# Kernel tuning notes

Hardware: AMD Instinct MI355X
Metric: run time of the kernel (lower is better)

The kernel has to match this reference:

```python
import math
import jax, jax.numpy as jnp
import numpy as np

FACTOR = 5

def setup_inputs() -> dict:
    key = jax.random.key(0)
    kq, kk, kv, ki = jax.random.split(key, 4)
    b, h, L, d = 4, 8, 4096, 64
    sample_k = min(L, int(FACTOR * math.log(L + 1)))  # 41
    q = jax.random.normal(kq, (b, h, L, d), dtype=jnp.float32)
    k = jax.random.normal(kk, (b, h, L, d), dtype=jnp.float32)
    v = jax.random.normal(kv, (b, h, L, d), dtype=jnp.float32)
    index_sample = jax.random.randint(ki, (L, sample_k), 0, L, dtype=jnp.int64)
    return {"q": q, "k": k, "v": v, "index_sample": index_sample}

def reference(q, k, v, index_sample):
    b, h, l_q, d = q.shape
    l_k = k.shape[2]
    n_top = min(l_q, int(FACTOR * math.log(l_q + 1)))
    # --- ProbSparse query selection ---
    # k_sample[b,h,q,s,d] = k[b,h,index_sample[q,s],d]  (avoids the O(lq*lk*d) expand)
    k_sample = k[:, :, index_sample, :]                      # (b,h,l_q,sample_k,d)
    qk_sample = jnp.einsum('bhqd,bhqsd->bhqs', q, k_sample)  # (b,h,l_q,sample_k)
    m = qk_sample.max(axis=-1) - qk_sample.mean(axis=-1)     # sparsity measure
    _, top_q = jax.lax.top_k(m, n_top)                       # (b,h,n_top)
    # --- sparse attention on selected queries ---
    q_reduce = jnp.take_along_axis(q, top_q[..., None], axis=2)  # (b,h,n_top,d)
    scale = 1.0 / math.sqrt(d)
    scores = jnp.einsum('bhnd,bhkd->bhnk', q_reduce, k) * scale
    attn = jax.nn.softmax(scores, axis=-1)
    context_top = jnp.einsum('bhnk,bhkd->bhnd', attn, v)
    # --- scatter into mean-initialized context (attn_mask is None path) ---
    context = jnp.broadcast_to(v.mean(axis=2, keepdims=True), (b, h, l_q, d))
    bi = jnp.arange(b)[:, None, None]
    hi = jnp.arange(h)[None, :, None]
    context = context.at[bi, hi, top_q].set(context_top)
    return context
```

## Files before the change

### kernel.cpp

```cpp
#include <hip/hip_runtime.h>
#include <hip/hip_bf16.h>


#define NTOP 41
#define NPAD 48
#define CH 64
#define CAND_CAP 64

typedef __attribute__((ext_vector_type(8))) short bf16x8;
typedef __attribute__((ext_vector_type(4))) float f32x4;

__device__ __forceinline__ unsigned short f2bf(float f) {
    unsigned int x = __float_as_uint(f);
    unsigned int r = (x + 0x7FFFu + ((x >> 16) & 1u)) >> 16;
    return (unsigned short)r;
}
__device__ __forceinline__ unsigned int pack2(float lo, float hi) {
    return ((unsigned int)f2bf(hi) << 16) | f2bf(lo);
}
__device__ __forceinline__ float dot8(const float4& qa, const float4& qb,
                                      const float4& ka, const float4& kb) {
    float p = 0.f;
    p = fmaf(qa.x, ka.x, p); p = fmaf(qa.y, ka.y, p);
    p = fmaf(qa.z, ka.z, p); p = fmaf(qa.w, ka.w, p);
    p = fmaf(qb.x, kb.x, p); p = fmaf(qb.y, kb.y, p);
    p = fmaf(qb.z, kb.z, p); p = fmaf(qb.w, kb.w, p);
    return p;
}
__device__ __forceinline__ float red8(float p) {
    p += __shfl_xor(p, 1);
    p += __shfl_xor(p, 2);
    p += __shfl_xor(p, 4);
    return p;
}

__global__ __launch_bounds__(256, 5) void K1_scores_vsum(const float* __restrict__ q,
                                                         const float* __restrict__ k,
                                                         const float* __restrict__ v,
                                                         const int* __restrict__ idxs,
                                                         float* __restrict__ m_out,
                                                         float* __restrict__ vpart) {
    __shared__ __align__(16) char smem[32 * 41 * 4 > 1024 ? 32 * 41 * 4 : 1024];
    int t = threadIdx.x;
    int bid = blockIdx.x;

    if (bid < 512) {
        float* red = (float*)smem;
        int bh = bid >> 4, chn = bid & 15;
        int d = t & 63, r = t >> 6;
        long long base = ((long long)bh << 12) + chn * 256;
        float acc = 0.f;
        for (int i = 0; i < 64; i++) acc += v[(base + i * 4 + r) * 64 + d];
        red[t] = acc;
        __syncthreads();
        if (r == 0)
            vpart[(bh * 16 + chn) * 64 + d] = red[d] + red[64 + d] + red[128 + d] + red[192 + d];
        return;
    }

    int* sidx = (int*)smem;
    int abid = bid - 512;
    int lane = t & 63, w = t >> 6;
    int g = lane >> 3, sl = lane & 7;
    int lb = ((abid & 7) << 9) + (abid >> 3);
    long long qflat = (long long)lb * 32 + w * 8 + g;
    int bh = (int)(qflat >> 12);
    int qi0 = (lb * 32) & 4095;
    for (int i = t; i < 32 * 41; i += 256)
        sidx[i] = idxs[(long long)qi0 * 41 + i] & 4095;
    const float4* q4 = (const float4*)q;
    const float4* k4 = (const float4*)k;
    float4 qa = q4[qflat * 16 + sl * 2];
    float4 qb = q4[qflat * 16 + sl * 2 + 1];
    long long kbase = ((long long)bh << 12) * 16;
    __syncthreads();
    const int* irow = sidx + (w * 8 + g) * 41;

    int k40 = irow[40];
    float4 ka40 = k4[kbase + (long long)k40 * 16 + sl * 2];
    float4 kb40 = k4[kbase + (long long)k40 * 16 + sl * 2 + 1];

    float maxv = -1e30f, sum = 0.f;
#pragma unroll
    for (int g8 = 0; g8 < 5; g8++) {
        int kis[8];
#pragma unroll
        for (int u = 0; u < 8; u++) kis[u] = irow[g8 * 8 + u];
        float4 ka[8], kb[8];
#pragma unroll
        for (int u = 0; u < 8; u++) {
            long long roff = kbase + (long long)kis[u] * 16 + sl * 2;
            ka[u] = k4[roff];
            kb[u] = k4[roff + 1];
        }
#pragma unroll
        for (int u = 0; u < 8; u++) {
            float p = red8(dot8(qa, qb, ka[u], kb[u]));
            maxv = fmaxf(maxv, p);
            sum += p;
        }
    }
    {
        float p = red8(dot8(qa, qb, ka40, kb40));
        maxv = fmaxf(maxv, p);
        sum += p;
    }
    if (sl == 0) m_out[qflat] = maxv - sum * (1.0f / 41.0f);
}

__global__ __launch_bounds__(256) void kB_topk(const float* __restrict__ m_in,
                                               int* __restrict__ topq) {
    __shared__ unsigned int uvals[4096];
    __shared__ unsigned int hist[256];
    __shared__ unsigned int scal[4];
    __shared__ int candIdx[CAND_CAP];
    __shared__ unsigned int candU[CAND_CAP];
    int bh = blockIdx.x, t = threadIdx.x;
    for (int i = t; i < 4096; i += 256) {
        unsigned int b = __float_as_uint(m_in[bh * 4096 + i]);
        uvals[i] = (b & 0x80000000u) ? ~b : (b | 0x80000000u);
    }
    hist[t] = 0;
    __syncthreads();
    for (int i = t; i < 4096; i += 256) atomicAdd(&hist[uvals[i] >> 24], 1u);
    __syncthreads();
    if (t == 0) {
        unsigned int cum = 0, b1 = 0, ca = 0;
        for (int j = 255; j >= 0; j--) {
            if (cum + hist[j] >= 41u) { b1 = (unsigned)j; ca = cum; break; }
            cum += hist[j];
        }
        scal[0] = b1; scal[1] = ca;
    }
    __syncthreads();
    unsigned int b1 = scal[0];
    hist[t] = 0;
    __syncthreads();
    for (int i = t; i < 4096; i += 256)
        if ((uvals[i] >> 24) == b1) atomicAdd(&hist[(uvals[i] >> 16) & 255u], 1u);
    __syncthreads();
    if (t == 0) {
        unsigned int cum = scal[1], b2 = 0;
        for (int j = 255; j >= 0; j--) {
            if (cum + hist[j] >= 41u) { b2 = (unsigned)j; break; }
            cum += hist[j];
        }
        scal[2] = (b1 << 24) | (b2 << 16);
        scal[3] = 0;
    }
    __syncthreads();
    unsigned int T = scal[2];
    for (int i = t; i < 4096; i += 256) {
        unsigned int u = uvals[i];
        if (u >= T) {
            unsigned int pos = atomicAdd(&scal[3], 1u);
            if (pos < CAND_CAP) { candIdx[pos] = i; candU[pos] = u; }
        }
    }
    __syncthreads();
    if (t < 64) {
        int n = (int)min(scal[3], (unsigned)CAND_CAP);
        unsigned int myU = (t < n) ? candU[t] : 0u;
        int myI = (t < n) ? candIdx[t] : 0x7fffffff;
        for (int it = 0; it < NTOP; it++) {
            unsigned int bu = myU;
            int bi = myI;
            for (int off = 32; off; off >>= 1) {
                unsigned int ou = __shfl_xor(bu, off);
                int oi = __shfl_xor(bi, off);
                if (ou > bu || (ou == bu && oi < bi)) { bu = ou; bi = oi; }
            }
            if (t == 0) topq[bh * NTOP + it] = bi;
            if (myI == bi) { myU = 0u; myI = 0x7fffffff; }
        }
    }
}

__global__ __launch_bounds__(256) void K3_attn_bcast(const float* __restrict__ q,
                                                     const float* __restrict__ k,
                                                     const float* __restrict__ v,
                                                     const int* __restrict__ topq,
                                                     const float* __restrict__ vpart,
                                                     float* __restrict__ part,
                                                     float* __restrict__ out,
                                                     int tiles, int tl) {
    __shared__ unsigned short qs[NPAD * 72];
    __shared__ unsigned short kb[CH * 72];
    __shared__ unsigned short vt[64 * 72];
    __shared__ unsigned short pb[NPAD * 72];
    __shared__ float sp[NPAD * 65];
    __shared__ float m_i[NPAD], l_i[NPAD], fac[NPAD];
    __shared__ __align__(16) float vm[64];

    const int t = threadIdx.x;
    const int bid = blockIdx.x;
    const int nE = tiles * 32;

    if (bid >= nE) {
        int gb = bid - nE;
        int bh = gb >> 6;
        if (t < 64) {
            float s = 0.f;
#pragma unroll
            for (int c = 0; c < 16; c++) s += vpart[(bh * 16 + c) * 64 + t];
            vm[t] = s * (1.0f / 4096.0f);
        }
        __syncthreads();
        long long g0 = (long long)gb * 1024 + t;
        float4* out4 = (float4*)out;
#pragma unroll
        for (int i = 0; i < 4; i++) {
            long long gg = g0 + i * 256;
            int d4 = (int)(gg & 15);
            out4[gg] = *(const float4*)(&vm[d4 * 4]);
        }
        return;
    }

    const int xcd = bid & 7, sub = (bid >> 3) & 3, tile = bid >> 5;
    const int bh = (xcd << 2) | sub;
    const int lane = t & 63, w = t >> 6;
    const int c = lane & 15, quad = lane >> 4;
    const long long bhbase = ((long long)bh) << 12;

    const float4* q4f = (const float4*)q;
    const float4* k4f = (const float4*)k;
    const float4* v4f = (const float4*)v;

    for (int i = t; i < NTOP * 16; i += 256) {
        int n = i >> 4, oc = i & 15;
        int row = topq[bh * NTOP + n];
        float4 val = q4f[(bhbase + row) * 16 + oc];
        uint2 pk;
        pk.x = pack2(val.x * 0.125f, val.y * 0.125f);
        pk.y = pack2(val.z * 0.125f, val.w * 0.125f);
        *(uint2*)(&qs[n * 72 + oc * 4]) = pk;
    }
    for (int i = t; i < 7 * 72; i += 256) {
        qs[NTOP * 72 + i] = 0;
        pb[NTOP * 72 + i] = 0;
    }
    if (t < NPAD) { m_i[t] = -1e30f; l_i[t] = 0.f; fac[t] = 0.f; }

    f32x4 oacc[3];
#pragma unroll
    for (int qt = 0; qt < 3; qt++) oacc[qt] = (f32x4){0.f, 0.f, 0.f, 0.f};

    const int l0 = tile * tl;
    const int nchunk = tl >> 6;
    for (int ch = 0; ch < nchunk; ch++) {
        const int lb = l0 + ch * CH;
        __syncthreads();
#pragma unroll
        for (int i = 0; i < 4; i++) {
            int idx = i * 256 + t;
            int j = idx >> 4, oc = idx & 15;
            float4 val = k4f[(bhbase + lb + j) * 16 + oc];
            uint2 pk;
            pk.x = pack2(val.x, val.y);
            pk.y = pack2(val.z, val.w);
            *(uint2*)(&kb[j * 72 + oc * 4]) = pk;
        }
        {
            int jp = t & 31, o = t >> 5;
            float4 a0 = v4f[(bhbase + lb + 2 * jp) * 16 + o * 2];
            float4 a1 = v4f[(bhbase + lb + 2 * jp) * 16 + o * 2 + 1];
            float4 b0 = v4f[(bhbase + lb + 2 * jp + 1) * 16 + o * 2];
            float4 b1 = v4f[(bhbase + lb + 2 * jp + 1) * 16 + o * 2 + 1];
            float av[8] = {a0.x, a0.y, a0.z, a0.w, a1.x, a1.y, a1.z, a1.w};
            float bv[8] = {b0.x, b0.y, b0.z, b0.w, b1.x, b1.y, b1.z, b1.w};
#pragma unroll
            for (int e = 0; e < 8; e++)
                *(unsigned int*)(&vt[(o * 8 + e) * 72 + 2 * jp]) = pack2(av[e], bv[e]);
        }
        __syncthreads();
        {
            const bf16x8 bk0 = *(const bf16x8*)(&kb[(w * 16 + c) * 72 + quad * 8]);
            const bf16x8 bk1 = *(const bf16x8*)(&kb[(w * 16 + c) * 72 + quad * 8 + 32]);
#pragma unroll
            for (int qt = 0; qt < 3; qt++) {
                const bf16x8 a0 = *(const bf16x8*)(&qs[(qt * 16 + c) * 72 + quad * 8]);
                const bf16x8 a1 = *(const bf16x8*)(&qs[(qt * 16 + c) * 72 + quad * 8 + 32]);
                f32x4 s4 = (f32x4){0.f, 0.f, 0.f, 0.f};
                s4 = __builtin_amdgcn_mfma_f32_16x16x32_bf16(a0, bk0, s4, 0, 0, 0);
                s4 = __builtin_amdgcn_mfma_f32_16x16x32_bf16(a1, bk1, s4, 0, 0, 0);
#pragma unroll
                for (int r = 0; r < 4; r++)
                    sp[(qt * 16 + quad * 4 + r) * 65 + w * 16 + c] = s4[r];
            }
        }
        __syncthreads();
        if (t < NTOP * 4) {
            int n = t >> 2, sub2 = t & 3;
            float rm = -1e30f;
#pragma unroll
            for (int j = 0; j < 16; j++) rm = fmaxf(rm, sp[n * 65 + sub2 * 16 + j]);
            rm = fmaxf(rm, __shfl_xor(rm, 1));
            rm = fmaxf(rm, __shfl_xor(rm, 2));
            float mo = m_i[n];
            float mn = fmaxf(mo, rm);
            float ssum = 0.f;
#pragma unroll
            for (int j = 0; j < 16; j += 2) {
                float e0 = __expf(sp[n * 65 + sub2 * 16 + j] - mn);
                float e1 = __expf(sp[n * 65 + sub2 * 16 + j + 1] - mn);
                ssum += e0 + e1;
                *(unsigned int*)(&pb[n * 72 + sub2 * 16 + j]) = pack2(e0, e1);
            }
            ssum += __shfl_xor(ssum, 1);
            ssum += __shfl_xor(ssum, 2);
            if (sub2 == 0) {
                float f = __expf(mo - mn);
                fac[n] = f;
                l_i[n] = l_i[n] * f + ssum;
                m_i[n] = mn;
            }
        }
        __syncthreads();
        {
            const bf16x8 bv0 = *(const bf16x8*)(&vt[(w * 16 + c) * 72 + quad * 8]);
            const bf16x8 bv1 = *(const bf16x8*)(&vt[(w * 16 + c) * 72 + quad * 8 + 32]);
#pragma unroll
            for (int qt = 0; qt < 3; qt++) {
                const bf16x8 a0 = *(const bf16x8*)(&pb[(qt * 16 + c) * 72 + quad * 8]);
                const bf16x8 a1 = *(const bf16x8*)(&pb[(qt * 16 + c) * 72 + quad * 8 + 32]);
                f32x4 o = oacc[qt];
                o.x *= fac[qt * 16 + quad * 4 + 0];
                o.y *= fac[qt * 16 + quad * 4 + 1];
                o.z *= fac[qt * 16 + quad * 4 + 2];
                o.w *= fac[qt * 16 + quad * 4 + 3];
                o = __builtin_amdgcn_mfma_f32_16x16x32_bf16(a0, bv0, o, 0, 0, 0);
                o = __builtin_amdgcn_mfma_f32_16x16x32_bf16(a1, bv1, o, 0, 0, 0);
                oacc[qt] = o;
            }
        }
    }
    __syncthreads();
    long long pbase = ((long long)(bh * tiles + tile)) * NTOP * 66;
    if (t < NTOP) {
        part[pbase + t * 66 + 0] = m_i[t];
        part[pbase + t * 66 + 1] = l_i[t];
    }
#pragma unroll
    for (int qt = 0; qt < 3; qt++) {
#pragma unroll
        for (int r = 0; r < 4; r++) {
            int n = qt * 16 + quad * 4 + r;
            if (n < NTOP) part[pbase + (long long)n * 66 + 2 + w * 16 + c] = oacc[qt][r];
        }
    }
}

__global__ __launch_bounds__(256) void kF_combine(const float* __restrict__ part,
                                                  const int* __restrict__ topq,
                                                  float* __restrict__ out, int tiles) {
    int t = threadIdx.x;
    int bh = blockIdx.x;
    int n = blockIdx.y * 4 + (t >> 6);
    int d = t & 63;
    if (n >= NTOP) return;
    long long base = ((long long)(bh * tiles)) * NTOP * 66 + (long long)n * 66;
    const long long ts = (long long)NTOP * 66;
    float M = -1e30f;
    for (int tt = 0; tt < tiles; tt++) M = fmaxf(M, part[base + tt * ts]);
    float L = 0.f, acc = 0.f;
    for (int tt = 0; tt < tiles; tt++) {
        float mt = part[base + tt * ts];
        float wgt = __expf(mt - M);
        L += part[base + tt * ts + 1] * wgt;
        acc += part[base + tt * ts + 2 + d] * wgt;
    }
    int row = topq[bh * NTOP + n];
    out[(((long long)bh << 12) + row) * 64 + d] = acc / L;
}

extern "C" void kernel_launch(void* const* d_in, const int* in_sizes, int n_in,
                              void* d_out, int out_size, void* d_ws, size_t ws_size,
                              hipStream_t stream) {
    const float* q = (const float*)d_in[0];
    const float* k = (const float*)d_in[1];
    const float* v = (const float*)d_in[2];
    const int* idxs = (const int*)d_in[3];
    float* out = (float*)d_out;

    char* ws = (char*)d_ws;
    float* ws_m = (float*)ws;
    int* ws_topq = (int*)(ws + 524288);
    float* ws_vpart = (float*)(ws + 532480);
    float* ws_part = (float*)(ws + 671744);

    size_t need16 = 671744ull + 16ull * 32 * NTOP * 66 * 4;
    int tiles = (ws_size >= need16) ? 16 : 8;
    int tl = 4096 / tiles;

    K1_scores_vsum<<<512 + 4096, 256, 0, stream>>>(q, k, v, idxs, ws_m, ws_vpart);
    kB_topk<<<32, 256, 0, stream>>>(ws_m, ws_topq);
    K3_attn_bcast<<<tiles * 32 + 2048, 256, 0, stream>>>(q, k, v, ws_topq, ws_vpart,
                                                         ws_part, out, tiles, tl);
    kF_combine<<<dim3(32, 11), 256, 0, stream>>>(ws_part, ws_topq, out, tiles);
}
```

Before: 256.7 us.

## Fuse top-k and combine into producer kernels via last-block atomic counters

Folds the top-k selection into the score kernel and the split-softmax combine into the attention kernel. Each uses a per-(b,h) atomic counter so the last finishing block does the dependent step, and a small init kernel zeroes the counters. The broadcast path now skips writing rows that the combine step will overwrite, which removes a write/overwrite race in the fused version. This cuts launch count and inter-kernel gaps, but serialises the top-k and combine work onto single tail blocks, and the score loop is restructured with smaller unrolling.

```diff
diff --git a/kernel.cpp b/kernel.cpp
--- a/kernel.cpp
+++ b/kernel.cpp
@@ -34,19 +34,27 @@
     return p;
 }
 
-__global__ __launch_bounds__(256, 5) void K1_scores_vsum(const float* __restrict__ q,
-                                                         const float* __restrict__ k,
-                                                         const float* __restrict__ v,
-                                                         const int* __restrict__ idxs,
-                                                         float* __restrict__ m_out,
-                                                         float* __restrict__ vpart) {
-    __shared__ __align__(16) char smem[32 * 41 * 4 > 1024 ? 32 * 41 * 4 : 1024];
-    int t = threadIdx.x;
-    int bid = blockIdx.x;
-
-    if (bid < 512) {
+__global__ void k0_init(unsigned int* __restrict__ cnt) {
+    if (threadIdx.x < 64) cnt[threadIdx.x] = 0u;
+}
+
+__global__ __launch_bounds__(256) void W1_scores(const float* __restrict__ q,
+                                                 const float* __restrict__ k,
+                                                 const float* __restrict__ v,
+                                                 const int* __restrict__ idxs,
+                                                 float* __restrict__ m_out,
+                                                 float* __restrict__ vpart,
+                                                 int* __restrict__ topq,
+                                                 unsigned int* __restrict__ cnt) {
+    __shared__ __align__(16) char smem[17952];
+    __shared__ int lastFlag;
+    const int t = threadIdx.x;
+    const int bid = blockIdx.x;
+
+    if (bid >= 4096) {
         float* red = (float*)smem;
-        int bh = bid >> 4, chn = bid & 15;
+        int cb = bid - 4096;
+        int bh = cb >> 4, chn = cb & 15;
         int d = t & 63, r = t >> 6;
         long long base = ((long long)bh << 12) + chn * 256;
         float acc = 0.f;
@@ -59,10 +67,9 @@
     }
 
     int* sidx = (int*)smem;
-    int abid = bid - 512;
     int lane = t & 63, w = t >> 6;
     int g = lane >> 3, sl = lane & 7;
-    int lb = ((abid & 7) << 9) + (abid >> 3);
+    int lb = ((bid & 7) << 9) + (bid >> 3);
     long long qflat = (long long)lb * 32 + w * 8 + g;
     int bh = (int)(qflat >> 12);
     int qi0 = (lb * 32) & 4095;
@@ -75,49 +82,54 @@
     long long kbase = ((long long)bh << 12) * 16;
     __syncthreads();
     const int* irow = sidx + (w * 8 + g) * 41;
-
-    int k40 = irow[40];
-    float4 ka40 = k4[kbase + (long long)k40 * 16 + sl * 2];
-    float4 kb40 = k4[kbase + (long long)k40 * 16 + sl * 2 + 1];
-
     float maxv = -1e30f, sum = 0.f;
-#pragma unroll
-    for (int g8 = 0; g8 < 5; g8++) {
-        int kis[8];
-#pragma unroll
-        for (int u = 0; u < 8; u++) kis[u] = irow[g8 * 8 + u];
-        float4 ka[8], kb[8];
-#pragma unroll
-        for (int u = 0; u < 8; u++) {
-            long long roff = kbase + (long long)kis[u] * 16 + sl * 2;
-            ka[u] = k4[roff];
-            kb[u] = k4[roff + 1];
-        }
-#pragma unroll
-        for (int u = 0; u < 8; u++) {
-            float p = red8(dot8(qa, qb, ka[u], kb[u]));
-            maxv = fmaxf(maxv, p);
-            sum += p;
-        }
+#pragma unroll 2
+    for (int g4 = 0; g4 < 10; g4++) {
+        int ki0 = irow[g4 * 4 + 0], ki1 = irow[g4 * 4 + 1];
+        int ki2 = irow[g4 * 4 + 2], ki3 = irow[g4 * 4 + 3];
+        float4 ka0 = k4[kbase + (long long)ki0 * 16 + sl * 2];
+        float4 kb0 = k4[kbase + (long long)ki0 * 16 + sl * 2 + 1];
+        float4 ka1 = k4[kbase + (long long)ki1 * 16 + sl * 2];
+        float4 kb1 = k4[kbase + (long long)ki1 * 16 + sl * 2 + 1];
+        float4 ka2 = k4[kbase + (long long)ki2 * 16 + sl * 2];
+        float4 kb2 = k4[kbase + (long long)ki2 * 16 + sl * 2 + 1];
+        float4 ka3 = k4[kbase + (long long)ki3 * 16 + sl * 2];
+        float4 kb3 = k4[kbase + (long long)ki3 * 16 + sl * 2 + 1];
+        float p0 = red8(dot8(qa, qb, ka0, kb0));
+        float p1 = red8(dot8(qa, qb, ka1, kb1));
+        float p2 = red8(dot8(qa, qb, ka2, kb2));
+        float p3 = red8(dot8(qa, qb, ka3, kb3));
+        maxv = fmaxf(maxv, fmaxf(fmaxf(p0, p1), fmaxf(p2, p3)));
+        sum += (p0 + p1) + (p2 + p3);
     }
     {
-        float p = red8(dot8(qa, qb, ka40, kb40));
+        int ki = irow[40];
+        float4 ka = k4[kbase + (long long)ki * 16 + sl * 2];
+        float4 kb = k4[kbase + (long long)ki * 16 + sl * 2 + 1];
+        float p = red8(dot8(qa, qb, ka, kb));
         maxv = fmaxf(maxv, p);
         sum += p;
     }
     if (sl == 0) m_out[qflat] = maxv - sum * (1.0f / 41.0f);
-}
-
-__global__ __launch_bounds__(256) void kB_topk(const float* __restrict__ m_in,
-                                               int* __restrict__ topq) {
-    __shared__ unsigned int uvals[4096];
-    __shared__ unsigned int hist[256];
-    __shared__ unsigned int scal[4];
-    __shared__ int candIdx[CAND_CAP];
-    __shared__ unsigned int candU[CAND_CAP];
-    int bh = blockIdx.x, t = threadIdx.x;
+
+    __syncthreads();
+    if (t == 0) {
+        __threadfence();
+        unsigned int o = atomicAdd(&cnt[bh], 1u);
+        lastFlag = (o == 127u);
+    }
+    __syncthreads();
+    if (!lastFlag) return;
+    __threadfence();
+
+    unsigned int* uvals = (unsigned int*)smem;
+    unsigned int* hist = (unsigned int*)(smem + 16384);
+    unsigned int* scal = (unsigned int*)(smem + 17408);
+    int* candIdx = (int*)(smem + 17424);
+    unsigned int* candU = (unsigned int*)(smem + 17680);
+
     for (int i = t; i < 4096; i += 256) {
-        unsigned int b = __float_as_uint(m_in[bh * 4096 + i]);
+        unsigned int b = __float_as_uint(m_out[bh * 4096 + i]);
         uvals[i] = (b & 0x80000000u) ? ~b : (b | 0x80000000u);
     }
     hist[t] = 0;
@@ -176,14 +188,15 @@
     }
 }
 
-__global__ __launch_bounds__(256) void K3_attn_bcast(const float* __restrict__ q,
-                                                     const float* __restrict__ k,
-                                                     const float* __restrict__ v,
-                                                     const int* __restrict__ topq,
-                                                     const float* __restrict__ vpart,
-                                                     float* __restrict__ part,
-                                                     float* __restrict__ out,
-                                                     int tiles, int tl) {
+__global__ __launch_bounds__(256) void W2_attn(const float* __restrict__ q,
+                                               const float* __restrict__ k,
+                                               const float* __restrict__ v,
+                                               const int* __restrict__ topq,
+                                               const float* __restrict__ vpart,
+                                               float* __restrict__ part,
+                                               float* __restrict__ out,
+                                               unsigned int* __restrict__ cnt,
+                                               int tiles, int tl) {
     __shared__ unsigned short qs[NPAD * 72];
     __shared__ unsigned short kb[CH * 72];
     __shared__ unsigned short vt[64 * 72];
@@ -191,6 +204,8 @@
     __shared__ float sp[NPAD * 65];
     __shared__ float m_i[NPAD], l_i[NPAD], fac[NPAD];
     __shared__ __align__(16) float vm[64];
+    __shared__ unsigned char flag[64];
+    __shared__ int lastFlag;
 
     const int t = threadIdx.x;
     const int bid = blockIdx.x;
@@ -204,6 +219,12 @@
 #pragma unroll
             for (int c = 0; c < 16; c++) s += vpart[(bh * 16 + c) * 64 + t];
             vm[t] = s * (1.0f / 4096.0f);
+            flag[t] = 0;
+        }
+        __syncthreads();
+        if (t < NTOP) {
+            int r = topq[bh * NTOP + t] - ((gb & 63) << 6);
+            if (r >= 0 && r < 64) flag[r] = 1;
         }
         __syncthreads();
         long long g0 = (long long)gb * 1024 + t;
@@ -211,8 +232,10 @@
 #pragma unroll
         for (int i = 0; i < 4; i++) {
             long long gg = g0 + i * 256;
-            int d4 = (int)(gg & 15);
-            out4[gg] = *(const float4*)(&vm[d4 * 4]);
+            if (!flag[(int)((gg >> 4) & 63)]) {
+                int d4 = (int)(gg & 15);
+                out4[gg] = *(const float4*)(&vm[d4 * 4]);
+            }
         }
         return;
     }
@@ -349,29 +372,35 @@
             if (n < NTOP) part[pbase + (long long)n * 66 + 2 + w * 16 + c] = oacc[qt][r];
         }
     }
-}
-
-__global__ __launch_bounds__(256) void kF_combine(const float* __restrict__ part,
-                                                  const int* __restrict__ topq,
-                                                  float* __restrict__ out, int tiles) {
-    int t = threadIdx.x;
-    int bh = blockIdx.x;
-    int n = blockIdx.y * 4 + (t >> 6);
-    int d = t & 63;
-    if (n >= NTOP) return;
-    long long base = ((long long)(bh * tiles)) * NTOP * 66 + (long long)n * 66;
+
+    __syncthreads();
+    if (t == 0) {
+        __threadfence();
+        unsigned int o = atomicAdd(&cnt[32 + bh], 1u);
+        lastFlag = (o == (unsigned)(tiles - 1));
+    }
+    __syncthreads();
+    if (!lastFlag) return;
+    __threadfence();
+
+    const int d = t & 63;
     const long long ts = (long long)NTOP * 66;
-    float M = -1e30f;
-    for (int tt = 0; tt < tiles; tt++) M = fmaxf(M, part[base + tt * ts]);
-    float L = 0.f, acc = 0.f;
-    for (int tt = 0; tt < tiles; tt++) {
-        float mt = part[base + tt * ts];
-        float wgt = __expf(mt - M);
-        L += part[base + tt * ts + 1] * wgt;
-        acc += part[base + tt * ts + 2 + d] * wgt;
-    }
-    int row = topq[bh * NTOP + n];
-    out[(((long long)bh << 12) + row) * 64 + d] = acc / L;
+    for (int bn = 0; bn < 44; bn += 4) {
+        int n = bn + (t >> 6);
+        if (n >= NTOP) break;
+        long long base = ((long long)(bh * tiles)) * ts + (long long)n * 66;
+        float M = -1e30f;
+        for (int tt = 0; tt < tiles; tt++) M = fmaxf(M, part[base + tt * ts]);
+        float L = 0.f, acc = 0.f;
+        for (int tt = 0; tt < tiles; tt++) {
+            float mt = part[base + tt * ts];
+            float wgt = __expf(mt - M);
+            L += part[base + tt * ts + 1] * wgt;
+            acc += part[base + tt * ts + 2 + d] * wgt;
+        }
+        int row = topq[bh * NTOP + n];
+        out[(((long long)bh << 12) + row) * 64 + d] = acc / L;
+    }
 }
 
 extern "C" void kernel_launch(void* const* d_in, const int* in_sizes, int n_in,
@@ -387,15 +416,16 @@
     float* ws_m = (float*)ws;
     int* ws_topq = (int*)(ws + 524288);
     float* ws_vpart = (float*)(ws + 532480);
+    unsigned int* ws_cnt = (unsigned int*)(ws + 663552);
     float* ws_part = (float*)(ws + 671744);
 
     size_t need16 = 671744ull + 16ull * 32 * NTOP * 66 * 4;
     int tiles = (ws_size >= need16) ? 16 : 8;
     int tl = 4096 / tiles;
 
-    K1_scores_vsum<<<512 + 4096, 256, 0, stream>>>(q, k, v, idxs, ws_m, ws_vpart);
-    kB_topk<<<32, 256, 0, stream>>>(ws_m, ws_topq);
-    K3_attn_bcast<<<tiles * 32 + 2048, 256, 0, stream>>>(q, k, v, ws_topq, ws_vpart,
-                                                         ws_part, out, tiles, tl);
-    kF_combine<<<dim3(32, 11), 256, 0, stream>>>(ws_part, ws_topq, out, tiles);
-}
+    k0_init<<<1, 64, 0, stream>>>(ws_cnt);
+    W1_scores<<<4096 + 512, 256, 0, stream>>>(q, k, v, idxs, ws_m, ws_vpart,
+                                              ws_topq, ws_cnt);
+    W2_attn<<<tiles * 32 + 2048, 256, 0, stream>>>(q, k, v, ws_topq, ws_vpart,
+                                                   ws_part, out, ws_cnt, tiles, tl);
+}
```

Result: slower. 529.3 us (+106.2%).
